# Kernel optimization log

Hardware: AMD Instinct MI355X
Metric: run time of the kernel (lower is better)

The kernel has to match this reference:

```python
import jax, jax.numpy as jnp
import numpy as np

N = 100000   # skill_num
D = 128      # skill_embed_dim
E = 500000   # edges per relation
S = 16384    # queried skills
NEG_SLOPE = 0.2


def _gat(x, edge_index, W, att_src, att_dst, bias):
    # PyG GATConv, heads=1, add_self_loops=True, eval mode (no dropout)
    n = x.shape[0]
    loops = jnp.arange(n)
    src = jnp.concatenate([edge_index[0], loops])
    dst = jnp.concatenate([edge_index[1], loops])
    h = x @ W                              # [N, D]
    a_src = h @ att_src                    # [N]
    a_dst = h @ att_dst                    # [N]
    e = jax.nn.leaky_relu(a_src[src] + a_dst[dst], NEG_SLOPE)  # [E+N]
    emax = jax.ops.segment_max(e, dst, num_segments=n)
    ex = jnp.exp(e - emax[dst])
    denom = jax.ops.segment_sum(ex, dst, num_segments=n)
    alpha = ex / (denom[dst] + 1e-16)
    out = jax.ops.segment_sum(alpha[:, None] * h[src], dst, num_segments=n)
    return out + bias


def _sage(x, edge_index, Wl, bl, Wr):
    # PyG SAGEConv, aggr='mean', root_weight=True (lin_r has no bias)
    n = x.shape[0]
    src, dst = edge_index[0], edge_index[1]
    ones = jnp.ones((src.shape[0],), dtype=x.dtype)
    deg = jax.ops.segment_sum(ones, dst, num_segments=n)
    agg = jax.ops.segment_sum(x[src], dst, num_segments=n)
    agg = agg / jnp.maximum(deg, 1.0)[:, None]
    return agg @ Wl + bl + x @ Wr


def setup_inputs() -> dict:
    key = jax.random.key(0)
    ks = jax.random.split(key, 16)
    sc = 1.0 / np.sqrt(D)
    inp = {
        "s": jax.random.randint(ks[0], (S,), 0, N),
        "t_s": 0,
        "t_e": 12,
        "ei_parent": jax.random.randint(ks[1], (2, E), 0, N),
        "ei_child": jax.random.randint(ks[2], (2, E), 0, N),
        "ei_relate": jax.random.randint(ks[3], (2, E), 0, N),
        "emb": jax.random.normal(ks[4], (N, D), dtype=jnp.float32),
        # GAT is_parent params
        "Wp": jax.random.normal(ks[5], (D, D), dtype=jnp.float32) * sc,
        "asp": jax.random.normal(ks[6], (D,), dtype=jnp.float32) * sc,
        "adp": jax.random.normal(ks[7], (D,), dtype=jnp.float32) * sc,
        "bp": jnp.zeros((D,), dtype=jnp.float32),
        # GAT is_child params
        "Wc": jax.random.normal(ks[8], (D, D), dtype=jnp.float32) * sc,
        "asc": jax.random.normal(ks[9], (D,), dtype=jnp.float32) * sc,
        "adc": jax.random.normal(ks[10], (D,), dtype=jnp.float32) * sc,
        "bc": jnp.zeros((D,), dtype=jnp.float32),
        # SAGE relate params
        "Wl": jax.random.normal(ks[11], (D, D), dtype=jnp.float32) * sc,
        "bl": jnp.zeros((D,), dtype=jnp.float32),
        "Wr": jax.random.normal(ks[12], (D, D), dtype=jnp.float32) * sc,
    }
    return inp


def reference(s, t_s, t_e, ei_parent, ei_child, ei_relate, emb,
              Wp, asp, adp, bp, Wc, asc, adc, bc, Wl, bl, Wr):
    out_parent = _gat(emb, ei_parent, Wp, asp, adp, bp)
    out_child = _gat(emb, ei_child, Wc, asc, adc, bc)
    out_relate = _sage(emb, ei_relate, Wl, bl, Wr)
    # HeteroConv(aggr='mean') over the three relation outputs
    node_out = (out_parent + out_child + out_relate) / 3.0
    return node_out[s, :]
```

## Files before the change

### kernel.cpp

```cpp
#include <hip/hip_runtime.h>

#define D 128
#define CAP 64
#define OVF_CAP 1024

typedef short bf16x8 __attribute__((ext_vector_type(8)));
typedef short short4v __attribute__((ext_vector_type(4)));
typedef float f32x4 __attribute__((ext_vector_type(4)));

__device__ __forceinline__ short f2bf(float f) {
  unsigned u = __builtin_bit_cast(unsigned, f);
  unsigned r = (u + 0x7fffu + ((u >> 16) & 1u)) >> 16;
  return (short)r;
}


__global__ void k_setup(const float* __restrict__ Wp, const float* __restrict__ asp,
                        const float* __restrict__ adp, const float* __restrict__ Wc,
                        const float* __restrict__ asc, const float* __restrict__ adc,
                        const float* __restrict__ bp, const float* __restrict__ bc,
                        const float* __restrict__ bl, const float* __restrict__ Wl,
                        const float* __restrict__ Wr,
                        float* __restrict__ v, short* __restrict__ wpack,
                        int* __restrict__ qid, int* __restrict__ counters,
                        int* __restrict__ deg3, int N, int S3) {
  int i = blockIdx.x * blockDim.x + threadIdx.x;
  int stride = gridDim.x * blockDim.x;
  for (int k = i; k < N; k += stride) qid[k] = -1;
  for (int k = i; k < S3; k += stride) deg3[k] = 0;
  if (i < 16) counters[i] = 0;

  for (int idx = i; idx < 16 * 8 * 64 * 8; idx += stride) {
    int j    = idx & 7;
    int lane = (idx >> 3) & 63;
    int nt   = (idx >> 9) & 7;
    int kt   = idx >> 12;
    int o = kt >> 2;
    int c = (kt & 3) * 32 + (lane >> 4) * 8 + j;
    int n = nt * 16 + (lane & 15);
    const float* W = (o == 0) ? Wp : (o == 1) ? Wc : (o == 2) ? Wl : Wr;
    wpack[idx] = f2bf(W[c * D + n]);
  }

  if (blockIdx.x == 0 && threadIdx.x < 128) {
    int k = threadIdx.x;
    float s0 = 0.f, s1 = 0.f, s2 = 0.f, s3 = 0.f;
    for (int d = 0; d < D; ++d) {
      float wp = Wp[k * D + d], wc = Wc[k * D + d];
      s0 += wp * asp[d]; s1 += wp * adp[d];
      s2 += wc * asc[d]; s3 += wc * adc[d];
    }
    v[k] = s0; v[D + k] = s1; v[2 * D + k] = s2; v[3 * D + k] = s3;
    v[4 * D + k] = bp[k] + bc[k] + bl[k];
  }
}

__global__ void k_pre(const int* __restrict__ s, int* __restrict__ qid,
                      int* __restrict__ uniq, int* __restrict__ counters, int S,
                      const float* __restrict__ emb, const float* __restrict__ v,
                      float* __restrict__ a_sp, float* __restrict__ a_dp,
                      float* __restrict__ a_sc, float* __restrict__ a_dc, int N) {
  int gtid = blockIdx.x * blockDim.x + threadIdx.x;
  if (gtid < S) {
    int n = s[gtid];
    if (atomicCAS(&qid[n], -1, -2) == -1) {
      int u = atomicAdd(&counters[0], 1);
      uniq[u] = n;
      qid[n] = u;
    }
  }
  int node = gtid >> 6;
  int lane = threadIdx.x & 63;
  if (node >= N) return;
  float2 x2 = ((const float2*)(emb + (size_t)node * D))[lane];
  float2 v0 = ((const float2*)(v))[lane];
  float2 v1 = ((const float2*)(v + D))[lane];
  float2 v2 = ((const float2*)(v + 2 * D))[lane];
  float2 v3 = ((const float2*)(v + 3 * D))[lane];
  float s0 = x2.x * v0.x + x2.y * v0.y;
  float s1 = x2.x * v1.x + x2.y * v1.y;
  float s2 = x2.x * v2.x + x2.y * v2.y;
  float s3 = x2.x * v3.x + x2.y * v3.y;
  for (int o = 32; o > 0; o >>= 1) {
    s0 += __shfl_down(s0, o);
    s1 += __shfl_down(s1, o);
    s2 += __shfl_down(s2, o);
    s3 += __shfl_down(s3, o);
  }
  if (lane == 0) { a_sp[node] = s0; a_dp[node] = s1; a_sc[node] = s2; a_dc[node] = s3; }
}

__global__ void __launch_bounds__(256) k_filter(
    const int* __restrict__ eiP, const int* __restrict__ eiC, const int* __restrict__ eiR,
    const int* __restrict__ qid,
    int* __restrict__ bktP, int* __restrict__ bktC, int* __restrict__ bktR,
    int* __restrict__ degP, int* __restrict__ degC, int* __restrict__ degR,
    int2* __restrict__ ovf, int* __restrict__ counters, int E) {
  int rel = blockIdx.y;
  const int* ei = (rel == 0) ? eiP : (rel == 1) ? eiC : eiR;
  int* bkt      = (rel == 0) ? bktP : (rel == 1) ? bktC : bktR;
  int* deg      = (rel == 0) ? degP : (rel == 1) ? degC : degR;
  int e = blockIdx.x * 256 + threadIdx.x;
  if (e >= E) return;
  int dst = ei[E + e];
  int u = qid[dst];
  if (u < 0) return;
  int src = ei[e];
  int pos = atomicAdd(&deg[u], 1);
  if (pos < CAP) {
    bkt[u * CAP + pos] = src;
  } else {
    int o = atomicAdd(&counters[4 + rel], 1);
    if (o < OVF_CAP) { int2 t; t.x = src; t.y = u; ovf[rel * OVF_CAP + o] = t; }
  }
}

__global__ void __launch_bounds__(256) k_accum(
    const int* __restrict__ bktP, const int* __restrict__ bktC, const int* __restrict__ bktR,
    const int* __restrict__ degP, const int* __restrict__ degC, const int* __restrict__ degR,
    const float* __restrict__ a_sp, const float* __restrict__ a_dp,
    const float* __restrict__ a_sc, const float* __restrict__ a_dc,
    const float* __restrict__ emb, const int* __restrict__ uniq,
    const int* __restrict__ counters, const int2* __restrict__ ovf,
    float* __restrict__ num_p, float* __restrict__ num_c, float* __restrict__ sum_r,
    float* __restrict__ den_p, float* __restrict__ den_c) {
  int U = counters[0];
  int u = blockIdx.x * 4 + (threadIdx.x >> 6);
  if (u >= U) return;
  int lane = threadIdx.x & 63;
  int rel = blockIdx.y;
  const int* bkt = (rel == 0) ? bktP : (rel == 1) ? bktC : bktR;
  const int* deg = (rel == 0) ? degP : (rel == 1) ? degC : degR;
  float* num     = (rel == 0) ? num_p : (rel == 1) ? num_c : sum_r;

  int m = deg[u];
  int mc = (m < CAP) ? m : CAP;
  int L = counters[4 + rel];
  const int* b0 = bkt + u * CAP;
  float2 acc; acc.x = 0.f; acc.y = 0.f;

  if (rel == 2) {
    for (int c = 0; c < mc; c += 64) {
      int mm = min(64, mc - c);
      int srcl = (lane < mm) ? b0[c + lane] : 0;
      for (int i = 0; i < mm; ++i) {
        int si = __shfl(srcl, i);
        float2 x2 = ((const float2*)(emb + (size_t)si * D))[lane];
        acc.x += x2.x; acc.y += x2.y;
      }
    }
    for (int l = 0; l < L; ++l) {
      int2 ov = ovf[2 * OVF_CAP + l];
      if (ov.y == u) {
        float2 x2 = ((const float2*)(emb + (size_t)ov.x * D))[lane];
        acc.x += x2.x; acc.y += x2.y;
      }
    }
  } else {
    const float* a_s = (rel == 0) ? a_sp : a_sc;
    const float* a_d = (rel == 0) ? a_dp : a_dc;
    int n = uniq[u];
    float adn = a_d[n];
    float denl = 0.f, denx = 0.f;
    for (int c = 0; c < mc; c += 64) {
      int mm = min(64, mc - c);
      int srcl = (lane < mm) ? b0[c + lane] : 0;
      float wl = 0.f;
      if (lane < mm) {
        float t = a_s[srcl] + adn;
        t = t >= 0.f ? t : 0.2f * t;
        wl = __expf(t);
      }
      denl += wl;
      for (int i = 0; i < mm; ++i) {
        int si = __shfl(srcl, i);
        float wi = __shfl(wl, i);
        float2 x2 = ((const float2*)(emb + (size_t)si * D))[lane];
        acc.x += wi * x2.x; acc.y += wi * x2.y;
      }
    }
    for (int l = 0; l < L; ++l) {
      int2 ov = ovf[rel * OVF_CAP + l];
      if (ov.y == u) {
        float t = a_s[ov.x] + adn;
        t = t >= 0.f ? t : 0.2f * t;
        float w = __expf(t);
        float2 x2 = ((const float2*)(emb + (size_t)ov.x * D))[lane];
        acc.x += w * x2.x; acc.y += w * x2.y;
        if (lane == 0) denx += w;
      }
    }
    for (int o = 32; o > 0; o >>= 1) denl += __shfl_down(denl, o);
    if (lane == 0) { ((rel == 0) ? den_p : den_c)[u] = denl + denx; }
  }
  ((float2*)(num + (size_t)u * D))[lane] = acc;
}

__global__ void __launch_bounds__(256) k_final(
    const float* __restrict__ num_p, const float* __restrict__ num_c,
    const float* __restrict__ sum_r, const float* __restrict__ emb,
    const int* __restrict__ uniq, const int* __restrict__ counters,
    const float* __restrict__ a_sp, const float* __restrict__ a_dp,
    const float* __restrict__ a_sc, const float* __restrict__ a_dc,
    const float* __restrict__ den_p, const float* __restrict__ den_c,
    const int* __restrict__ deg_r, const float* __restrict__ vvec,
    const short* __restrict__ wpack, float* __restrict__ outU) {
  __shared__ short A_lds[16 * 64 * 8];
  int U = counters[0];
  int u0 = blockIdx.x * 16;
  if (u0 >= U) return;
  int tid = threadIdx.x;

  {
    int m = tid >> 4;
    int oc = tid & 15;
    int u = u0 + m;
    int uu = (u < U) ? u : u0;
    int n = uniq[uu];
    float tP = a_sp[n] + a_dp[n]; tP = tP >= 0.f ? tP : 0.2f * tP;
    float wP = __expf(tP);
    float rP = 1.f / (den_p[uu] + wP);
    float tC = a_sc[n] + a_dc[n]; tC = tC >= 0.f ? tC : 0.2f * tC;
    float wC = __expf(tC);
    float rC = 1.f / (den_c[uu] + wC);
    float dg = (float)deg_r[uu]; if (dg < 1.f) dg = 1.f;
    float rdeg = 1.f / dg;
#pragma unroll
    for (int half = 0; half < 2; ++half) {
      int c4 = oc * 8 + half * 4;
      int q = (c4 >> 3) & 3;
      int j0 = c4 & 7;
      int ktc = c4 >> 5;
      float4 e4  = *(const float4*)(emb   + (size_t)n  * D + c4);
      float4 np4 = *(const float4*)(num_p + (size_t)uu * D + c4);
      float4 nc4 = *(const float4*)(num_c + (size_t)uu * D + c4);
      float4 sr4 = *(const float4*)(sum_r + (size_t)uu * D + c4);
      float4 z[4];
      z[0].x = (np4.x + wP * e4.x) * rP; z[0].y = (np4.y + wP * e4.y) * rP;
      z[0].z = (np4.z + wP * e4.z) * rP; z[0].w = (np4.w + wP * e4.w) * rP;
      z[1].x = (nc4.x + wC * e4.x) * rC; z[1].y = (nc4.y + wC * e4.y) * rC;
      z[1].z = (nc4.z + wC * e4.z) * rC; z[1].w = (nc4.w + wC * e4.w) * rC;
      z[2].x = sr4.x * rdeg; z[2].y = sr4.y * rdeg;
      z[2].z = sr4.z * rdeg; z[2].w = sr4.w * rdeg;
      z[3] = e4;
#pragma unroll
      for (int o = 0; o < 4; ++o) {
        int kt = o * 4 + ktc;
        short4v s4;
        s4.x = f2bf(z[o].x); s4.y = f2bf(z[o].y);
        s4.z = f2bf(z[o].z); s4.w = f2bf(z[o].w);
        *(short4v*)&A_lds[(kt * 64 + q * 16 + m) * 8 + j0] = s4;
      }
    }
  }
  __syncthreads();

  int w = tid >> 6;
  int lane = tid & 63;
  f32x4 acc0 = {0.f, 0.f, 0.f, 0.f};
  f32x4 acc1 = {0.f, 0.f, 0.f, 0.f};
  const bf16x8* wp = (const bf16x8*)wpack;
#pragma unroll
  for (int kt = 0; kt < 16; ++kt) {
    bf16x8 a  = *(const bf16x8*)&A_lds[(kt * 64 + lane) * 8];
    bf16x8 b0 = wp[(kt * 8 + 2 * w) * 64 + lane];
    bf16x8 b1 = wp[(kt * 8 + 2 * w + 1) * 64 + lane];
    acc0 = __builtin_amdgcn_mfma_f32_16x16x32_bf16(a, b0, acc0, 0, 0, 0);
    acc1 = __builtin_amdgcn_mfma_f32_16x16x32_bf16(a, b1, acc1, 0, 0, 0);
  }

  int col0 = 2 * w * 16 + (lane & 15);
  int col1 = col0 + 16;
  int r0 = (lane >> 4) * 4;
  float b0v = vvec[4 * D + col0] * (1.f / 3.f);
  float b1v = vvec[4 * D + col1] * (1.f / 3.f);
#pragma unroll
  for (int reg = 0; reg < 4; ++reg) {
    int u = u0 + r0 + reg;
    if (u < U) {
      outU[(size_t)u * D + col0] = acc0[reg] * (1.f / 3.f) + b0v;
      outU[(size_t)u * D + col1] = acc1[reg] * (1.f / 3.f) + b1v;
    }
  }
}

__global__ void k_gather(const int* __restrict__ s, const int* __restrict__ qid,
                         const float* __restrict__ outU, float* __restrict__ out, int S) {
  int idx = blockIdx.x * blockDim.x + threadIdx.x;
  if (idx >= S * D) return;
  int i = idx >> 7;
  int d = idx & (D - 1);
  int u = qid[s[i]];
  out[idx] = outU[(size_t)u * D + d];
}


extern "C" void kernel_launch(void* const* d_in, const int* in_sizes, int n_in,
                              void* d_out, int out_size, void* d_ws, size_t ws_size,
                              hipStream_t stream) {
  const int*   s   = (const int*)d_in[0];
  const int*   eip = (const int*)d_in[3];
  const int*   eic = (const int*)d_in[4];
  const int*   eir = (const int*)d_in[5];
  const float* emb = (const float*)d_in[6];
  const float* Wp  = (const float*)d_in[7];
  const float* asp = (const float*)d_in[8];
  const float* adp = (const float*)d_in[9];
  const float* bp  = (const float*)d_in[10];
  const float* Wc  = (const float*)d_in[11];
  const float* asc = (const float*)d_in[12];
  const float* adc = (const float*)d_in[13];
  const float* bc  = (const float*)d_in[14];
  const float* Wl  = (const float*)d_in[15];
  const float* bl  = (const float*)d_in[16];
  const float* Wr  = (const float*)d_in[17];
  float* out = (float*)d_out;

  const int S = in_sizes[0];
  const int E = in_sizes[3] / 2;
  const int N = in_sizes[6] / D;

  char* base = (char*)d_ws;
  size_t off = 0;
  auto carve = [&](size_t bytes) -> char* {
    char* q = base + off;
    off += (bytes + 255) & ~(size_t)255;
    return q;
  };
  float* a_sp     = (float*)carve((size_t)N * 4);
  float* a_dp     = (float*)carve((size_t)N * 4);
  float* a_sc     = (float*)carve((size_t)N * 4);
  float* a_dc     = (float*)carve((size_t)N * 4);
  int*   qid      = (int*)carve((size_t)N * 4);
  int*   uniq     = (int*)carve((size_t)S * 4);
  int*   counters = (int*)carve(64);
  float* vvec     = (float*)carve(5 * D * 4);
  short* wpack    = (short*)carve((size_t)16 * 8 * 64 * 8 * 2);
  float* num_p    = (float*)carve((size_t)S * D * 4);
  float* den_p    = (float*)carve((size_t)S * 4);
  float* num_c    = (float*)carve((size_t)S * D * 4);
  float* den_c    = (float*)carve((size_t)S * 4);
  float* sum_r    = (float*)carve((size_t)S * D * 4);
  float* outU     = (float*)carve((size_t)S * D * 4);
  int*   degP     = (int*)carve((size_t)S * 4);
  int*   degC     = (int*)carve((size_t)S * 4);
  int*   degR     = (int*)carve((size_t)S * 4);
  int*   bktP     = (int*)carve((size_t)S * CAP * 4);
  int*   bktC     = (int*)carve((size_t)S * CAP * 4);
  int*   bktR     = (int*)carve((size_t)S * CAP * 4);
  int2*  ovf      = (int2*)carve((size_t)3 * OVF_CAP * 8);
  (void)ws_size; (void)n_in; (void)out_size;

  k_setup<<<256, 256, 0, stream>>>(Wp, asp, adp, Wc, asc, adc, bp, bc, bl, Wl, Wr,
                                   vvec, wpack, qid, counters, degP, N, 3 * S);

  k_pre<<<(N * 64 + 255) / 256, 256, 0, stream>>>(s, qid, uniq, counters, S,
                                                  emb, vvec, a_sp, a_dp, a_sc, a_dc, N);

  k_filter<<<dim3((E + 255) / 256, 3), 256, 0, stream>>>(
      eip, eic, eir, qid, bktP, bktC, bktR, degP, degC, degR, ovf, counters, E);

  k_accum<<<dim3((S + 3) / 4, 3), 256, 0, stream>>>(
      bktP, bktC, bktR, degP, degC, degR,
      a_sp, a_dp, a_sc, a_dc, emb, uniq, counters, ovf,
      num_p, num_c, sum_r, den_p, den_c);

  k_final<<<(S + 15) / 16, 256, 0, stream>>>(num_p, num_c, sum_r, emb, uniq, counters,
                                             a_sp, a_dp, a_sc, a_dc, den_p, den_c, degR,
                                             vvec, wpack, outU);
  k_gather<<<(S * D + 255) / 256, 256, 0, stream>>>(s, qid, outU, out, S);
}
```

Before: 218.9 us.

## Gather neighbor embeddings from a bf16 copy with a 4-way unrolled loop

k_pre now writes a bf16-packed copy of the embedding table, and k_accum gathers neighbor rows from that copy instead of the fp32 table. This halves the bytes of the random-access gathers. The edge loop is restructured into a single pass over the bucket, unrolled by four so several loads are in flight, and SAGE is treated as the weighted case with unit weights. The cost is an extra 25.6MB write in k_pre and reduced precision in the aggregated sums. It also adds a clamp of the overflow count.

```diff
diff --git a/kernel.cpp b/kernel.cpp
--- a/kernel.cpp
+++ b/kernel.cpp
@@ -12,6 +12,12 @@
   unsigned u = __builtin_bit_cast(unsigned, f);
   unsigned r = (u + 0x7fffu + ((u >> 16) & 1u)) >> 16;
   return (short)r;
+}
+__device__ __forceinline__ float bflo(unsigned r) {
+  return __builtin_bit_cast(float, r << 16);
+}
+__device__ __forceinline__ float bfhi(unsigned r) {
+  return __builtin_bit_cast(float, r & 0xffff0000u);
 }
 
 
@@ -59,7 +65,8 @@
                       int* __restrict__ uniq, int* __restrict__ counters, int S,
                       const float* __restrict__ emb, const float* __restrict__ v,
                       float* __restrict__ a_sp, float* __restrict__ a_dp,
-                      float* __restrict__ a_sc, float* __restrict__ a_dc, int N) {
+                      float* __restrict__ a_sc, float* __restrict__ a_dc,
+                      unsigned* __restrict__ ebf, int N) {
   int gtid = blockIdx.x * blockDim.x + threadIdx.x;
   if (gtid < S) {
     int n = s[gtid];
@@ -73,6 +80,9 @@
   int lane = threadIdx.x & 63;
   if (node >= N) return;
   float2 x2 = ((const float2*)(emb + (size_t)node * D))[lane];
+  unsigned p = ((unsigned)(unsigned short)f2bf(x2.x)) |
+               (((unsigned)(unsigned short)f2bf(x2.y)) << 16);
+  ebf[(size_t)node * 64 + lane] = p;
   float2 v0 = ((const float2*)(v))[lane];
   float2 v1 = ((const float2*)(v + D))[lane];
   float2 v2 = ((const float2*)(v + 2 * D))[lane];
@@ -120,7 +130,7 @@
     const int* __restrict__ degP, const int* __restrict__ degC, const int* __restrict__ degR,
     const float* __restrict__ a_sp, const float* __restrict__ a_dp,
     const float* __restrict__ a_sc, const float* __restrict__ a_dc,
-    const float* __restrict__ emb, const int* __restrict__ uniq,
+    const unsigned* __restrict__ ebf, const int* __restrict__ uniq,
     const int* __restrict__ counters, const int2* __restrict__ ovf,
     float* __restrict__ num_p, float* __restrict__ num_c, float* __restrict__ sum_r,
     float* __restrict__ den_p, float* __restrict__ den_c) {
@@ -136,62 +146,76 @@
   int m = deg[u];
   int mc = (m < CAP) ? m : CAP;
   int L = counters[4 + rel];
+  if (L > OVF_CAP) L = OVF_CAP;
   const int* b0 = bkt + u * CAP;
   float2 acc; acc.x = 0.f; acc.y = 0.f;
 
-  if (rel == 2) {
-    for (int c = 0; c < mc; c += 64) {
-      int mm = min(64, mc - c);
-      int srcl = (lane < mm) ? b0[c + lane] : 0;
-      for (int i = 0; i < mm; ++i) {
-        int si = __shfl(srcl, i);
-        float2 x2 = ((const float2*)(emb + (size_t)si * D))[lane];
-        acc.x += x2.x; acc.y += x2.y;
-      }
-    }
-    for (int l = 0; l < L; ++l) {
-      int2 ov = ovf[2 * OVF_CAP + l];
-      if (ov.y == u) {
-        float2 x2 = ((const float2*)(emb + (size_t)ov.x * D))[lane];
-        acc.x += x2.x; acc.y += x2.y;
-      }
-    }
-  } else {
+  int srcl = (lane < mc) ? b0[lane] : 0;
+  float wl = 0.f;
+  bool gat = (rel != 2);
+  float denl = 0.f;
+  if (gat) {
     const float* a_s = (rel == 0) ? a_sp : a_sc;
     const float* a_d = (rel == 0) ? a_dp : a_dc;
     int n = uniq[u];
     float adn = a_d[n];
-    float denl = 0.f, denx = 0.f;
-    for (int c = 0; c < mc; c += 64) {
-      int mm = min(64, mc - c);
-      int srcl = (lane < mm) ? b0[c + lane] : 0;
-      float wl = 0.f;
-      if (lane < mm) {
-        float t = a_s[srcl] + adn;
-        t = t >= 0.f ? t : 0.2f * t;
-        wl = __expf(t);
-      }
-      denl += wl;
-      for (int i = 0; i < mm; ++i) {
-        int si = __shfl(srcl, i);
-        float wi = __shfl(wl, i);
-        float2 x2 = ((const float2*)(emb + (size_t)si * D))[lane];
-        acc.x += wi * x2.x; acc.y += wi * x2.y;
-      }
-    }
+    if (lane < mc) {
+      float t = a_s[srcl] + adn;
+      t = t >= 0.f ? t : 0.2f * t;
+      wl = __expf(t);
+    }
+    denl = wl;
+  } else {
+    wl = (lane < mc) ? 1.f : 0.f;
+  }
+
+  int i = 0;
+  for (; i + 4 <= mc; i += 4) {
+    int s0 = __shfl(srcl, i),     s1 = __shfl(srcl, i + 1);
+    int s2 = __shfl(srcl, i + 2), s3 = __shfl(srcl, i + 3);
+    float w0 = __shfl(wl, i),     w1 = __shfl(wl, i + 1);
+    float w2 = __shfl(wl, i + 2), w3 = __shfl(wl, i + 3);
+    unsigned r0 = ebf[(size_t)s0 * 64 + lane];
+    unsigned r1 = ebf[(size_t)s1 * 64 + lane];
+    unsigned r2 = ebf[(size_t)s2 * 64 + lane];
+    unsigned r3 = ebf[(size_t)s3 * 64 + lane];
+    acc.x += w0 * bflo(r0) + w1 * bflo(r1) + w2 * bflo(r2) + w3 * bflo(r3);
+    acc.y += w0 * bfhi(r0) + w1 * bfhi(r1) + w2 * bfhi(r2) + w3 * bfhi(r3);
+  }
+  for (; i < mc; ++i) {
+    int si = __shfl(srcl, i);
+    float wi = __shfl(wl, i);
+    unsigned r = ebf[(size_t)si * 64 + lane];
+    acc.x += wi * bflo(r);
+    acc.y += wi * bfhi(r);
+  }
+
+  if (gat) {
+    const float* a_s = (rel == 0) ? a_sp : a_sc;
+    const float* a_d = (rel == 0) ? a_dp : a_dc;
+    float adn = a_d[uniq[u]];
+    float denx = 0.f;
     for (int l = 0; l < L; ++l) {
       int2 ov = ovf[rel * OVF_CAP + l];
       if (ov.y == u) {
         float t = a_s[ov.x] + adn;
         t = t >= 0.f ? t : 0.2f * t;
         float w = __expf(t);
-        float2 x2 = ((const float2*)(emb + (size_t)ov.x * D))[lane];
-        acc.x += w * x2.x; acc.y += w * x2.y;
+        unsigned r = ebf[(size_t)ov.x * 64 + lane];
+        acc.x += w * bflo(r); acc.y += w * bfhi(r);
         if (lane == 0) denx += w;
       }
     }
     for (int o = 32; o > 0; o >>= 1) denl += __shfl_down(denl, o);
     if (lane == 0) { ((rel == 0) ? den_p : den_c)[u] = denl + denx; }
+  } else {
+    for (int l = 0; l < L; ++l) {
+      int2 ov = ovf[2 * OVF_CAP + l];
+      if (ov.y == u) {
+        unsigned r = ebf[(size_t)ov.x * 64 + lane];
+        acc.x += bflo(r); acc.y += bfhi(r);
+      }
+    }
   }
   ((float2*)(num + (size_t)u * D))[lane] = acc;
 }
@@ -327,42 +351,44 @@
     off += (bytes + 255) & ~(size_t)255;
     return q;
   };
-  float* a_sp     = (float*)carve((size_t)N * 4);
-  float* a_dp     = (float*)carve((size_t)N * 4);
-  float* a_sc     = (float*)carve((size_t)N * 4);
-  float* a_dc     = (float*)carve((size_t)N * 4);
-  int*   qid      = (int*)carve((size_t)N * 4);
-  int*   uniq     = (int*)carve((size_t)S * 4);
-  int*   counters = (int*)carve(64);
-  float* vvec     = (float*)carve(5 * D * 4);
-  short* wpack    = (short*)carve((size_t)16 * 8 * 64 * 8 * 2);
-  float* num_p    = (float*)carve((size_t)S * D * 4);
-  float* den_p    = (float*)carve((size_t)S * 4);
-  float* num_c    = (float*)carve((size_t)S * D * 4);
-  float* den_c    = (float*)carve((size_t)S * 4);
-  float* sum_r    = (float*)carve((size_t)S * D * 4);
-  float* outU     = (float*)carve((size_t)S * D * 4);
-  int*   degP     = (int*)carve((size_t)S * 4);
-  int*   degC     = (int*)carve((size_t)S * 4);
-  int*   degR     = (int*)carve((size_t)S * 4);
-  int*   bktP     = (int*)carve((size_t)S * CAP * 4);
-  int*   bktC     = (int*)carve((size_t)S * CAP * 4);
-  int*   bktR     = (int*)carve((size_t)S * CAP * 4);
-  int2*  ovf      = (int2*)carve((size_t)3 * OVF_CAP * 8);
+  float*    a_sp     = (float*)carve((size_t)N * 4);
+  float*    a_dp     = (float*)carve((size_t)N * 4);
+  float*    a_sc     = (float*)carve((size_t)N * 4);
+  float*    a_dc     = (float*)carve((size_t)N * 4);
+  int*      qid      = (int*)carve((size_t)N * 4);
+  unsigned* ebf      = (unsigned*)carve((size_t)N * 64 * 4);
+  int*      uniq     = (int*)carve((size_t)S * 4);
+  int*      counters = (int*)carve(64);
+  float*    vvec     = (float*)carve(5 * D * 4);
+  short*    wpack    = (short*)carve((size_t)16 * 8 * 64 * 8 * 2);
+  float*    num_p    = (float*)carve((size_t)S * D * 4);
+  float*    den_p    = (float*)carve((size_t)S * 4);
+  float*    num_c    = (float*)carve((size_t)S * D * 4);
+  float*    den_c    = (float*)carve((size_t)S * 4);
+  float*    sum_r    = (float*)carve((size_t)S * D * 4);
+  float*    outU     = (float*)carve((size_t)S * D * 4);
+  int*      degP     = (int*)carve((size_t)S * 4);
+  int*      degC     = (int*)carve((size_t)S * 4);
+  int*      degR     = (int*)carve((size_t)S * 4);
+  int*      bktP     = (int*)carve((size_t)S * CAP * 4);
+  int*      bktC     = (int*)carve((size_t)S * CAP * 4);
+  int*      bktR     = (int*)carve((size_t)S * CAP * 4);
+  int2*     ovf      = (int2*)carve((size_t)3 * OVF_CAP * 8);
   (void)ws_size; (void)n_in; (void)out_size;
 
   k_setup<<<256, 256, 0, stream>>>(Wp, asp, adp, Wc, asc, adc, bp, bc, bl, Wl, Wr,
                                    vvec, wpack, qid, counters, degP, N, 3 * S);
 
   k_pre<<<(N * 64 + 255) / 256, 256, 0, stream>>>(s, qid, uniq, counters, S,
-                                                  emb, vvec, a_sp, a_dp, a_sc, a_dc, N);
+                                                  emb, vvec, a_sp, a_dp, a_sc, a_dc,
+                                                  ebf, N);
 
   k_filter<<<dim3((E + 255) / 256, 3), 256, 0, stream>>>(
       eip, eic, eir, qid, bktP, bktC, bktR, degP, degC, degR, ovf, counters, E);
 
   k_accum<<<dim3((S + 3) / 4, 3), 256, 0, stream>>>(
       bktP, bktC, bktR, degP, degC, degR,
-      a_sp, a_dp, a_sc, a_dc, emb, uniq, counters, ovf,
+      a_sp, a_dp, a_sc, a_dc, ebf, uniq, counters, ovf,
       num_p, num_c, sum_r, den_p, den_c);
 
   k_final<<<(S + 15) / 16, 256, 0, stream>>>(num_p, num_c, sum_r, emb, uniq, counters,
```

Measured after the change: 213.2 us. 2.6% less time.
